# Kernel tuning notes

Measured on AMD Instinct MI355X. Metric: run time of the kernel, lower is better.

Reference implementation:

```python
import jax, jax.numpy as jnp
import numpy as np

NUM_EMBEDDINGS = 16384
EMBED_DIM = 2048
B, C, H, W = 8, EMBED_DIM, 32, 32


def setup_inputs() -> dict:
    key = jax.random.key(0)
    k1, k2 = jax.random.split(key)
    hidden_state = jax.random.normal(k1, (B, C, H, W), dtype=jnp.float32)
    embedding = jax.random.normal(k2, (NUM_EMBEDDINGS, EMBED_DIM), dtype=jnp.float32)
    return {"hidden_state": hidden_state, "embedding": embedding}


def _l2_normalize(x, axis=-1, eps=1e-12):
    # matches torch F.normalize(p=2): x / max(||x||, eps)
    n = jnp.sqrt(jnp.sum(x * x, axis=axis, keepdims=True))
    return x / jnp.maximum(n, eps)


def reference(hidden_state, embedding):
    b, c, h, w = hidden_state.shape
    # (B,C,H,W) -> (B*H*W, C)
    flat = jnp.transpose(hidden_state, (0, 2, 3, 1)).reshape(-1, c)
    z = _l2_normalize(flat)                      # [N, D]
    e = _l2_normalize(embedding)                 # [K, D]
    sim = jnp.matmul(z, e.T)                     # [N, K]
    idx = jnp.argmax(sim, axis=1)                # [N]
    quant = e[idx]                               # [N, D]
    quant = quant.reshape(b, h, w, c).transpose(0, 3, 1, 2)
    return quant, idx
```

## Files before the change

### kernel.cpp

```cpp
#include <hip/hip_runtime.h>
#include <hip/hip_bf16.h>

#define NQ   8192
#define NK   16384
#define DIM  2048
#define KTILES 128
#define QUANT_ELEMS (8*2048*32*32)

typedef __attribute__((ext_vector_type(8))) short bf16x8;
typedef __attribute__((ext_vector_type(4))) float f32x4;

__device__ __forceinline__ void async16(const void* g, void* lds) {
  __builtin_amdgcn_global_load_lds(
      (const __attribute__((address_space(1))) unsigned int*)g,
      (__attribute__((address_space(3))) unsigned int*)lds,
      16, 0, 0);
}

__device__ __forceinline__ void t2_add(float v, int i,
                                       float& v1, int& i1, float& v2, int& i2) {
  if (v > v1) { v2 = v1; i2 = i1; v1 = v; i1 = i; }
  else if (v > v2) { v2 = v; i2 = i; }
}

__global__ __launch_bounds__(256) void norm_e_kernel(
    const float* __restrict__ e, __hip_bfloat16* __restrict__ eh,
    float* __restrict__ enorm) {
  const int k = blockIdx.x;
  const int t = threadIdx.x;
  const float* row = e + (size_t)k * DIM;
  float v[8];
  double ss = 0.0;
#pragma unroll
  for (int j = 0; j < 8; j++) { v[j] = row[t + 256 * j]; ss += (double)v[j] * (double)v[j]; }
  for (int s = 32; s; s >>= 1) ss += __shfl_down(ss, s);
  __shared__ double sb[4];
  __shared__ float snorm;
  if ((t & 63) == 0) sb[t >> 6] = ss;
  __syncthreads();
  if (t == 0) {
    snorm = fmaxf((float)sqrt(sb[0] + sb[1] + sb[2] + sb[3]), 1e-12f);
    enorm[k] = snorm;
  }
  __syncthreads();
  const float nf = snorm;
#pragma unroll
  for (int j = 0; j < 8; j++)
    eh[(size_t)k * DIM + t + 256 * j] = __float2bfloat16(v[j] / nf);
}

__global__ __launch_bounds__(256) void norm_z_kernel(
    const float* __restrict__ hid, __hip_bfloat16* __restrict__ zh) {
  const int bh = blockIdx.x;
  const int b = bh >> 5, h = bh & 31;
  const int n0 = bh * 32;
  const int t = threadIdx.x;
  const int w = t & 31, cp = t >> 5;

  __shared__ double ssq[8][32];
  __shared__ float nrm[32];
  __shared__ float tile[32][65];

  double acc = 0.0;
  const float* base = hid + ((size_t)b * DIM) * 1024 + h * 32 + w;
#pragma unroll 8
  for (int k = 0; k < 256; k++) {
    float val = base[(size_t)(cp * 256 + k) * 1024];
    acc += (double)val * (double)val;
  }
  ssq[cp][w] = acc;
  __syncthreads();
  if (t < 32) {
    double s = 0.0;
#pragma unroll
    for (int j = 0; j < 8; j++) s += ssq[j][t];
    nrm[t] = fmaxf((float)sqrt(s), 1e-12f);
  }
  __syncthreads();

  for (int ct = 0; ct < 32; ct++) {
    const int c0 = ct * 64;
#pragma unroll
    for (int jt = 0; jt < 8; jt++) {
      const int cl = jt * 8 + cp;
      tile[w][cl] = base[(size_t)(c0 + cl) * 1024];
    }
    __syncthreads();
#pragma unroll
    for (int it = 0; it < 8; it++) {
      const int nl = it * 4 + (t >> 6);
      const int cl = t & 63;
      zh[(size_t)(n0 + nl) * DIM + c0 + cl] =
          __float2bfloat16(tile[nl][cl] / nrm[nl]);
    }
    __syncthreads();
  }
}

__global__ __launch_bounds__(512, 2) void gemm_top2(
    const __hip_bfloat16* __restrict__ A, const __hip_bfloat16* __restrict__ B,
    float4* __restrict__ pertile ) {
  __shared__ __align__(16) __hip_bfloat16 As[2][256 * 64];
  __shared__ __align__(16) __hip_bfloat16 Bs[2][256 * 64];

  const int nb = blockIdx.x;
  const int kb = blockIdx.y;
  const int n0 = nb * 256;
  const int k0 = kb * 256;

  const int tid  = threadIdx.x;
  const int wid  = tid >> 6;
  const int lane = tid & 63;
  const int wm = wid >> 2;
  const int wn = wid & 3;

  const int lr = lane >> 3;
  const int sc = ((lane & 7) ^ lr) * 8;
  const int srow = wid * 8 + lr;

  f32x4 acc[8][4];
#pragma unroll
  for (int i = 0; i < 8; i++)
#pragma unroll
    for (int j = 0; j < 4; j++) acc[i][j] = (f32x4){0.f, 0.f, 0.f, 0.f};

#define STAGE(bufi, d0_)                                                      \
  do {                                                                        \
    _Pragma("unroll")                                                         \
    for (int q = 0; q < 4; q++) {                                             \
      const int row = q * 64 + srow;                                          \
      async16(A + (size_t)(n0 + row) * DIM + (d0_) + sc,                      \
              (char*)As[bufi] + q * 8192 + wid * 1024);                       \
      async16(B + (size_t)(k0 + row) * DIM + (d0_) + sc,                      \
              (char*)Bs[bufi] + q * 8192 + wid * 1024);                       \
    }                                                                         \
  } while (0)

#define COMPUTE(bufi)                                                         \
  do {                                                                        \
    _Pragma("unroll")                                                         \
    for (int kk = 0; kk < 2; kk++) {                                          \
      bf16x8 af[8], bfr[4];                                                   \
      const int cg = kk * 4 + (lane >> 4);                                    \
      _Pragma("unroll")                                                       \
      for (int mi = 0; mi < 8; mi++) {                                        \
        int r = wm * 128 + mi * 16 + (lane & 15);                             \
        af[mi] = *(const bf16x8*)(As[bufi] + r * 64 + ((cg ^ (r & 7)) * 8));  \
      }                                                                       \
      _Pragma("unroll")                                                       \
      for (int ni = 0; ni < 4; ni++) {                                        \
        int r = wn * 64 + ni * 16 + (lane & 15);                              \
        bfr[ni] = *(const bf16x8*)(Bs[bufi] + r * 64 + ((cg ^ (r & 7)) * 8)); \
      }                                                                       \
      _Pragma("unroll")                                                       \
      for (int mi = 0; mi < 8; mi++)                                          \
        _Pragma("unroll")                                                     \
        for (int ni = 0; ni < 4; ni++)                                        \
          acc[mi][ni] = __builtin_amdgcn_mfma_f32_16x16x32_bf16(              \
              af[mi], bfr[ni], acc[mi][ni], 0, 0, 0);                         \
    }                                                                         \
  } while (0)

  STAGE(0, 0);
  __syncthreads();
  for (int i = 0; i < 15; i++) {
    const int d0 = i * 128;
    STAGE(1, d0 + 64);
    COMPUTE(0);
    __syncthreads();
    STAGE(0, d0 + 128);
    COMPUTE(1);
    __syncthreads();
  }
  STAGE(1, 1984);
  COMPUTE(0);
  __syncthreads();
  COMPUTE(1);
#undef STAGE
#undef COMPUTE

  __syncthreads();
  float4* buf = (float4*)As;
  const int cbase = k0 + wn * 64 + (lane & 15);
#pragma unroll
  for (int mi = 0; mi < 8; mi++) {
#pragma unroll
    for (int j = 0; j < 4; j++) {
      float v1 = -INFINITY, v2 = -INFINITY;
      int i1 = -1, i2 = -1;
#pragma unroll
      for (int ni = 0; ni < 4; ni++)
        t2_add(acc[mi][ni][j], cbase + ni * 16, v1, i1, v2, i2);
      for (int s = 1; s < 16; s <<= 1) {
        float ov1 = __shfl_xor(v1, s); int oi1 = __shfl_xor(i1, s);
        float ov2 = __shfl_xor(v2, s); int oi2 = __shfl_xor(i2, s);
        t2_add(ov1, oi1, v1, i1, v2, i2);
        t2_add(ov2, oi2, v1, i1, v2, i2);
      }
      if ((lane & 15) == 0) {
        int rl = wm * 128 + mi * 16 + ((lane >> 4) << 2) + j;
        buf[rl * 4 + wn] = make_float4(v1, v2, __int_as_float(i1), __int_as_float(i2));
      }
    }
  }
  __syncthreads();
  {
    const int row = tid >> 1, half = tid & 1;
    float4 a = buf[row * 4 + half * 2 + 0], b = buf[row * 4 + half * 2 + 1];
    float v1 = a.x, v2 = a.y;
    int i1 = __float_as_int(a.z), i2 = __float_as_int(a.w);
    t2_add(b.x, __float_as_int(b.z), v1, i1, v2, i2);
    t2_add(b.y, __float_as_int(b.w), v1, i1, v2, i2);
    pertile[(size_t)(n0 + row) * KTILES + kb * 2 + half] =
        make_float4(v1, v2, __int_as_float(i1), __int_as_float(i2));
  }
}

#define DELTA 2e-3f
__global__ __launch_bounds__(256) void rescore_kernel(
    const float4* __restrict__ pertile, const float* __restrict__ hid,
    const float* __restrict__ emb, float* __restrict__ idx_f,
    int* __restrict__ idx_i) {
  const int n = blockIdx.x;
  const int t = threadIdx.x;
  __shared__ double sredd[2][4];
  __shared__ float sm[4];
  __shared__ int sl[128];
  __shared__ int scnt;

  float4 e4 = (t < 128) ? pertile[(size_t)n * KTILES + t]
                        : make_float4(-INFINITY, -INFINITY, 0.f, 0.f);
  float m = e4.x;
  for (int s = 32; s; s >>= 1) m = fmaxf(m, __shfl_xor(m, s));
  if ((t & 63) == 0) sm[t >> 6] = m;
  __syncthreads();
  if (t == 0) {
    sm[0] = fmaxf(fmaxf(sm[0], sm[1]), fmaxf(sm[2], sm[3]));
    scnt = 0;
  }
  __syncthreads();
  const float thr = sm[0] - DELTA;
  if (t < 128) {
    if (e4.x >= thr) { int p = atomicAdd(&scnt, 1); if (p < 128) sl[p] = __float_as_int(e4.z); }
    if (e4.y >= thr) { int p = atomicAdd(&scnt, 1); if (p < 128) sl[p] = __float_as_int(e4.w); }
  }
  __syncthreads();
  const int cnt = min(scnt, 128);

  const int b = n >> 10, hw = n & 1023;
  const float* zbase = hid + (size_t)b * DIM * 1024 + hw;
  double zv[8];
#pragma unroll
  for (int j = 0; j < 8; j++) zv[j] = (double)zbase[(size_t)(t + 256 * j) * 1024];

  double bestv = -1e300;
  int besti = 0x7fffffff;
  for (int c = 0; c < cnt; c++) {
    const int k = sl[c];
    const float* erow = emb + (size_t)k * DIM;
    double dot = 0.0, ee = 0.0;
#pragma unroll
    for (int j = 0; j < 8; j++) {
      double ev = (double)erow[t + 256 * j];
      dot += zv[j] * ev;
      ee  += ev * ev;
    }
    for (int s = 32; s; s >>= 1) { dot += __shfl_down(dot, s); ee += __shfl_down(ee, s); }
    if ((t & 63) == 0) { sredd[0][t >> 6] = dot; sredd[1][t >> 6] = ee; }
    __syncthreads();
    if (t == 0) {
      double td = sredd[0][0] + sredd[0][1] + sredd[0][2] + sredd[0][3];
      double te = sredd[1][0] + sredd[1][1] + sredd[1][2] + sredd[1][3];
      double sim = td / sqrt(te);
      if (sim > bestv || (sim == bestv && k < besti)) { bestv = sim; besti = k; }
    }
    __syncthreads();
  }
  if (t == 0) { idx_f[n] = (float)besti; idx_i[n] = besti; }
}

__global__ __launch_bounds__(256) void gather_kernel(
    const float* __restrict__ emb, const float* __restrict__ enorm,
    const int* __restrict__ idx, float* __restrict__ out) {
  const int bh = blockIdx.x;
  const int b = bh >> 5, h = bh & 31;
  const int n0 = bh * 32;
  const int c0 = blockIdx.y * 64;
  const int t = threadIdx.x;

  __shared__ int rows[32];
  __shared__ float nrm[32];
  __shared__ float tile[32][65];

  if (t < 32) {
    int r = idx[n0 + t];
    rows[t] = r;
    nrm[t] = enorm[r];
  }
  __syncthreads();
#pragma unroll
  for (int it = 0; it < 8; it++) {
    const int nl = it * 4 + (t >> 6);
    const int cl = t & 63;
    tile[nl][cl] = emb[(size_t)rows[nl] * DIM + c0 + cl] / nrm[nl];
  }
  __syncthreads();
#pragma unroll
  for (int jt = 0; jt < 8; jt++) {
    const int cl = jt * 8 + (t >> 5);
    const int w = t & 31;
    out[((size_t)(b * DIM + c0 + cl) << 10) + (h << 5) + w] = tile[w][cl];
  }
}

extern "C" void kernel_launch(void* const* d_in, const int* in_sizes, int n_in,
                              void* d_out, int out_size, void* d_ws, size_t ws_size,
                              hipStream_t stream) {
  const float* hidden = (const float*)d_in[0];
  const float* emb    = (const float*)d_in[1];
  float* out = (float*)d_out;

  char* ws = (char*)d_ws;
  __hip_bfloat16* eh = (__hip_bfloat16*)ws; ws += (size_t)NK * DIM * 2;
  __hip_bfloat16* zh = (__hip_bfloat16*)ws; ws += (size_t)NQ * DIM * 2;
  float4* pertile = (float4*)ws;            ws += (size_t)NQ * KTILES * 16;
  float* enorm = (float*)ws;                ws += (size_t)NK * 4;
  int* idxi = (int*)ws;                     ws += (size_t)NQ * 4;

  norm_e_kernel<<<NK, 256, 0, stream>>>(emb, eh, enorm);
  norm_z_kernel<<<256, 256, 0, stream>>>(hidden, zh);
  gemm_top2<<<dim3(NQ / 256, NK / 256), 512, 0, stream>>>(zh, eh, pertile);
  rescore_kernel<<<NQ, 256, 0, stream>>>(pertile, hidden, emb, out + QUANT_ELEMS, idxi);
  gather_kernel<<<dim3(256, DIM / 64), 256, 0, stream>>>(emb, enorm, idxi, out);
}
```

Baseline: 2.097 ms.

## Interleave staged global loads with quarter-tile MFMA phases in GEMM main loop

Restructures the bf16 GEMM main loop into four sub-phases per K-tile. Each phase loads a slice of A fragments from LDS, issues part of the next tile's async global-to-LDS copies, then runs a block of MFMAs at raised wave priority. Explicit vmcnt/lgkmcnt waits and raw barriers replace full __syncthreads. The intent is finer-grained overlap of memory traffic with matrix math and lower register pressure from holding fewer A fragments at once. The cost is many more barriers, and hand-tuned wait counts that must match the load order exactly.

```diff
diff --git a/kernel.cpp b/kernel.cpp
--- a/kernel.cpp
+++ b/kernel.cpp
@@ -116,7 +116,12 @@
 
   const int lr = lane >> 3;
   const int sc = ((lane & 7) ^ lr) * 8;
-  const int srow = wid * 8 + lr;
+
+  const int la15 = lane & 15;
+  const int rba  = wm * 128 + la15;
+  const int rbb  = wn * 64 + la15;
+  const int slot0 = (((lane >> 4) ^ (lane & 7)) * 8);
+  const int slot1 = (((4 + (lane >> 4)) ^ (lane & 7)) * 8);
 
   f32x4 acc[8][4];
 #pragma unroll
@@ -124,60 +129,128 @@
 #pragma unroll
     for (int j = 0; j < 4; j++) acc[i][j] = (f32x4){0.f, 0.f, 0.f, 0.f};
 
-#define STAGE(bufi, d0_)                                                      \
+  bf16x8 af[2][2];
+  bf16x8 bfr[4][2];
+
+#define STAGE_BU(BUF, d0_, h)                                                 \
   do {                                                                        \
     _Pragma("unroll")                                                         \
-    for (int q = 0; q < 4; q++) {                                             \
-      const int row = q * 64 + srow;                                          \
-      async16(A + (size_t)(n0 + row) * DIM + (d0_) + sc,                      \
-              (char*)As[bufi] + q * 8192 + wid * 1024);                       \
-      async16(B + (size_t)(k0 + row) * DIM + (d0_) + sc,                      \
-              (char*)Bs[bufi] + q * 8192 + wid * 1024);                       \
+    for (int j_ = 0; j_ < 2; j_++) {                                          \
+      const int row_ = (h) * 128 + j_ * 64 + wid * 8 + lr;                    \
+      async16(B + (size_t)(k0 + row_) * DIM + (d0_) + sc,                     \
+              (char*)&Bs[BUF][0] + (h) * 16384 + j_ * 8192 + wid * 1024);     \
     }                                                                         \
   } while (0)
 
-#define COMPUTE(bufi)                                                         \
+#define STAGE_A1(BUF, d0_, i_)                                                \
+  do {                                                                        \
+    const int row_ = (wid < 4) ? ((i_) * 32 + wid * 8 + lr)                   \
+                               : (128 + (i_) * 32 + (wid - 4) * 8 + lr);      \
+    const int lb_  = (wid < 4) ? ((i_) * 4096 + wid * 1024)                   \
+                               : (16384 + (i_) * 4096 + (wid - 4) * 1024);    \
+    async16(A + (size_t)(n0 + row_) * DIM + (d0_) + sc,                       \
+            (char*)&As[BUF][0] + lb_);                                        \
+  } while (0)
+
+#define AF_LOAD(BUF, q)                                                       \
   do {                                                                        \
     _Pragma("unroll")                                                         \
-    for (int kk = 0; kk < 2; kk++) {                                          \
-      bf16x8 af[8], bfr[4];                                                   \
-      const int cg = kk * 4 + (lane >> 4);                                    \
+    for (int m_ = 0; m_ < 2; m_++) {                                          \
+      af[m_][0] = *(const bf16x8*)(&As[BUF][(rba + (q)*32 + m_*16)*64 + slot0]); \
+      af[m_][1] = *(const bf16x8*)(&As[BUF][(rba + (q)*32 + m_*16)*64 + slot1]); \
+    }                                                                         \
+  } while (0)
+
+#define BF_LOAD(BUF)                                                          \
+  do {                                                                        \
+    _Pragma("unroll")                                                         \
+    for (int n_ = 0; n_ < 4; n_++) {                                          \
+      bfr[n_][0] = *(const bf16x8*)(&Bs[BUF][(rbb + n_*16)*64 + slot0]);      \
+      bfr[n_][1] = *(const bf16x8*)(&Bs[BUF][(rbb + n_*16)*64 + slot1]);      \
+    }                                                                         \
+  } while (0)
+
+#define MFMA_Q(q)                                                             \
+  do {                                                                        \
+    __builtin_amdgcn_s_setprio(1);                                            \
+    _Pragma("unroll")                                                         \
+    for (int kk_ = 0; kk_ < 2; kk_++)                                         \
       _Pragma("unroll")                                                       \
-      for (int mi = 0; mi < 8; mi++) {                                        \
-        int r = wm * 128 + mi * 16 + (lane & 15);                             \
-        af[mi] = *(const bf16x8*)(As[bufi] + r * 64 + ((cg ^ (r & 7)) * 8));  \
-      }                                                                       \
-      _Pragma("unroll")                                                       \
-      for (int ni = 0; ni < 4; ni++) {                                        \
-        int r = wn * 64 + ni * 16 + (lane & 15);                              \
-        bfr[ni] = *(const bf16x8*)(Bs[bufi] + r * 64 + ((cg ^ (r & 7)) * 8)); \
-      }                                                                       \
-      _Pragma("unroll")                                                       \
-      for (int mi = 0; mi < 8; mi++)                                          \
+      for (int m_ = 0; m_ < 2; m_++)                                          \
         _Pragma("unroll")                                                     \
-        for (int ni = 0; ni < 4; ni++)                                        \
-          acc[mi][ni] = __builtin_amdgcn_mfma_f32_16x16x32_bf16(              \
-              af[mi], bfr[ni], acc[mi][ni], 0, 0, 0);                         \
-    }                                                                         \
-  } while (0)
-
-  STAGE(0, 0);
-  __syncthreads();
+        for (int n_ = 0; n_ < 4; n_++)                                        \
+          acc[(q)*2 + m_][n_] = __builtin_amdgcn_mfma_f32_16x16x32_bf16(      \
+              af[m_][kk_], bfr[n_][kk_], acc[(q)*2 + m_][n_], 0, 0, 0);       \
+    __builtin_amdgcn_s_setprio(0);                                            \
+  } while (0)
+
+#define LGKM0 asm volatile("s_waitcnt lgkmcnt(0)" ::: "memory")
+#define BAR   __builtin_amdgcn_s_barrier()
+#define SB0   __builtin_amdgcn_sched_barrier(0)
+
+#define TILE_MAIN(BUF, d0n_)                                                  \
+  do {                                                                        \
+                                                                      \
+    asm volatile("s_waitcnt vmcnt(2)" ::: "memory");                          \
+    BAR;                                                                      \
+    BF_LOAD(BUF); AF_LOAD(BUF, 0);                                            \
+    STAGE_BU(1 - (BUF), (d0n_), 0);                                           \
+    LGKM0; MFMA_Q(0); BAR;                                                    \
+                                                                      \
+    BAR;                                                                      \
+    AF_LOAD(BUF, 1);                                                          \
+    STAGE_BU(1 - (BUF), (d0n_), 1);                                           \
+    LGKM0; MFMA_Q(1); BAR;                                                    \
+                                                                      \
+    asm volatile("s_waitcnt vmcnt(4)" ::: "memory");                          \
+    BAR;                                                                      \
+    AF_LOAD(BUF, 2);                                                          \
+    STAGE_A1(1 - (BUF), (d0n_), 0); STAGE_A1(1 - (BUF), (d0n_), 1);           \
+    LGKM0; MFMA_Q(2); BAR;                                                    \
+                                                                      \
+    BAR;                                                                      \
+    AF_LOAD(BUF, 3);                                                          \
+    STAGE_A1(1 - (BUF), (d0n_), 2); STAGE_A1(1 - (BUF), (d0n_), 3);           \
+    LGKM0; MFMA_Q(3); BAR;                                                    \
+  } while (0)
+
+#define TILE_LAST(BUF)                                                        \
+  do {                                                                        \
+    asm volatile("s_waitcnt vmcnt(2)" ::: "memory");                          \
+    BAR;                                                                      \
+    BF_LOAD(BUF); AF_LOAD(BUF, 0); LGKM0; MFMA_Q(0); BAR;                     \
+    BAR;                                                                      \
+    AF_LOAD(BUF, 1); LGKM0; MFMA_Q(1); BAR;                                   \
+    asm volatile("s_waitcnt vmcnt(0)" ::: "memory");                          \
+    BAR;                                                                      \
+    AF_LOAD(BUF, 2); LGKM0; MFMA_Q(2); BAR;                                   \
+    BAR;                                                                      \
+    AF_LOAD(BUF, 3); LGKM0; MFMA_Q(3); BAR;                                   \
+  } while (0)
+
+  STAGE_BU(0, 0, 0); SB0;
+  STAGE_BU(0, 0, 1); SB0;
+  STAGE_A1(0, 0, 0); STAGE_A1(0, 0, 1); SB0;
+  STAGE_A1(0, 0, 2); STAGE_A1(0, 0, 3);
+
+#pragma unroll 1
   for (int i = 0; i < 15; i++) {
-    const int d0 = i * 128;
-    STAGE(1, d0 + 64);
-    COMPUTE(0);
-    __syncthreads();
-    STAGE(0, d0 + 128);
-    COMPUTE(1);
-    __syncthreads();
-  }
-  STAGE(1, 1984);
-  COMPUTE(0);
-  __syncthreads();
-  COMPUTE(1);
-#undef STAGE
-#undef COMPUTE
+    TILE_MAIN(0, i * 128 + 64);
+    TILE_MAIN(1, i * 128 + 128);
+  }
+  TILE_MAIN(0, 1984);
+  TILE_LAST(1);
+
+#undef TILE_MAIN
+#undef TILE_LAST
+#undef STAGE_BU
+#undef STAGE_A1
+#undef AF_LOAD
+#undef BF_LOAD
+#undef MFMA_Q
+#undef LGKM0
+#undef BAR
+#undef SB0
 
   __syncthreads();
   float4* buf = (float4*)As;
```

After: 1.843 ms. 1.14x faster.

## Halve GEMM K-slab to 32, raise occupancy, use fine-grained vmcnt waits

Applied to the files above, without the earlier changes.

Cuts the per-stage K slab from 64 to 32 so LDS per block halves, and raises launch bounds to 4 blocks per CU. The swizzle is reworked for the narrower rows, and full __syncthreads is replaced by explicit s_waitcnt vmcnt plus s_barrier with sched_barriers. MFMA sections also get setprio, so loads for the next stage overlap compute. The aim is more latency hiding through occupancy and less synchronisation stall. The cost is twice as many barriers per K, and register pressure with 128 accumulator floats at 4 blocks of 512 threads may cause spills.

```diff
diff --git a/kernel.cpp b/kernel.cpp
--- a/kernel.cpp
+++ b/kernel.cpp
@@ -97,11 +97,11 @@
   }
 }
 
-__global__ __launch_bounds__(512, 2) void gemm_top2(
+__global__ __launch_bounds__(512, 4) void gemm_top2(
     const __hip_bfloat16* __restrict__ A, const __hip_bfloat16* __restrict__ B,
     float4* __restrict__ pertile ) {
-  __shared__ __align__(16) __hip_bfloat16 As[2][256 * 64];
-  __shared__ __align__(16) __hip_bfloat16 Bs[2][256 * 64];
+  __shared__ __align__(16) __hip_bfloat16 As[2][256 * 32];
+  __shared__ __align__(16) __hip_bfloat16 Bs[2][256 * 32];
 
   const int nb = blockIdx.x;
   const int kb = blockIdx.y;
@@ -114,9 +114,9 @@
   const int wm = wid >> 2;
   const int wn = wid & 3;
 
-  const int lr = lane >> 3;
-  const int sc = ((lane & 7) ^ lr) * 8;
-  const int srow = wid * 8 + lr;
+  const int la15 = lane & 15;
+  const int slotE = (((lane >> 4) ^ (la15 & 3)) * 8);
+  const int scol = (((lane & 3) ^ ((lane >> 2) & 3)) * 8);
 
   f32x4 acc[8][4];
 #pragma unroll
@@ -124,60 +124,71 @@
 #pragma unroll
     for (int j = 0; j < 4; j++) acc[i][j] = (f32x4){0.f, 0.f, 0.f, 0.f};
 
-#define STAGE(bufi, d0_)                                                      \
+#define STAGE(BUF, d0_)                                                       \
   do {                                                                        \
     _Pragma("unroll")                                                         \
-    for (int q = 0; q < 4; q++) {                                             \
-      const int row = q * 64 + srow;                                          \
-      async16(A + (size_t)(n0 + row) * DIM + (d0_) + sc,                      \
-              (char*)As[bufi] + q * 8192 + wid * 1024);                       \
-      async16(B + (size_t)(k0 + row) * DIM + (d0_) + sc,                      \
-              (char*)Bs[bufi] + q * 8192 + wid * 1024);                       \
+    for (int q_ = 0; q_ < 2; q_++) {                                          \
+      const int row_ = q_ * 128 + wid * 16 + (lane >> 2);                     \
+      async16(A + (size_t)(n0 + row_) * DIM + (d0_) + scol,                   \
+              (char*)&As[BUF][0] + q_ * 8192 + wid * 1024);                   \
+      async16(B + (size_t)(k0 + row_) * DIM + (d0_) + scol,                   \
+              (char*)&Bs[BUF][0] + q_ * 8192 + wid * 1024);                   \
     }                                                                         \
   } while (0)
 
-#define COMPUTE(bufi)                                                         \
+#define COMPUTE(BUF)                                                          \
   do {                                                                        \
+    bf16x8 af[8], bfr[4];                                                     \
     _Pragma("unroll")                                                         \
-    for (int kk = 0; kk < 2; kk++) {                                          \
-      bf16x8 af[8], bfr[4];                                                   \
-      const int cg = kk * 4 + (lane >> 4);                                    \
+    for (int mi = 0; mi < 8; mi++)                                            \
+      af[mi] = *(const bf16x8*)(&As[BUF][(wm * 128 + mi * 16 + la15) * 32 + slotE]); \
+    _Pragma("unroll")                                                         \
+    for (int ni = 0; ni < 4; ni++)                                            \
+      bfr[ni] = *(const bf16x8*)(&Bs[BUF][(wn * 64 + ni * 16 + la15) * 32 + slotE]); \
+    __builtin_amdgcn_s_setprio(1);                                            \
+    _Pragma("unroll")                                                         \
+    for (int mi = 0; mi < 8; mi++)                                            \
       _Pragma("unroll")                                                       \
-      for (int mi = 0; mi < 8; mi++) {                                        \
-        int r = wm * 128 + mi * 16 + (lane & 15);                             \
-        af[mi] = *(const bf16x8*)(As[bufi] + r * 64 + ((cg ^ (r & 7)) * 8));  \
-      }                                                                       \
-      _Pragma("unroll")                                                       \
-      for (int ni = 0; ni < 4; ni++) {                                        \
-        int r = wn * 64 + ni * 16 + (lane & 15);                              \
-        bfr[ni] = *(const bf16x8*)(Bs[bufi] + r * 64 + ((cg ^ (r & 7)) * 8)); \
-      }                                                                       \
-      _Pragma("unroll")                                                       \
-      for (int mi = 0; mi < 8; mi++)                                          \
-        _Pragma("unroll")                                                     \
-        for (int ni = 0; ni < 4; ni++)                                        \
-          acc[mi][ni] = __builtin_amdgcn_mfma_f32_16x16x32_bf16(              \
-              af[mi], bfr[ni], acc[mi][ni], 0, 0, 0);                         \
-    }                                                                         \
+      for (int ni = 0; ni < 4; ni++)                                          \
+        acc[mi][ni] = __builtin_amdgcn_mfma_f32_16x16x32_bf16(                \
+            af[mi], bfr[ni], acc[mi][ni], 0, 0, 0);                           \
+    __builtin_amdgcn_s_setprio(0);                                            \
   } while (0)
 
+#define VMCNT4 asm volatile("s_waitcnt vmcnt(4)" ::: "memory")
+#define VMCNT0 asm volatile("s_waitcnt vmcnt(0)" ::: "memory")
+#define BAR    __builtin_amdgcn_s_barrier()
+#define SB0    __builtin_amdgcn_sched_barrier(0)
+
   STAGE(0, 0);
-  __syncthreads();
-  for (int i = 0; i < 15; i++) {
-    const int d0 = i * 128;
-    STAGE(1, d0 + 64);
+#pragma unroll 1
+  for (int i = 0; i < 31; i++) {
+    const int d0 = i * 64;
+    STAGE(1, d0 + 32);
+    VMCNT4;
+    BAR; SB0;
     COMPUTE(0);
-    __syncthreads();
-    STAGE(0, d0 + 128);
+    BAR; SB0;
+    STAGE(0, d0 + 64);
+    VMCNT4;
+    BAR; SB0;
     COMPUTE(1);
-    __syncthreads();
-  }
-  STAGE(1, 1984);
+    BAR; SB0;
+  }
+  STAGE(1, 2016);
+  VMCNT4;
+  BAR; SB0;
   COMPUTE(0);
-  __syncthreads();
+  VMCNT0;
+  BAR; SB0;
   COMPUTE(1);
+
 #undef STAGE
 #undef COMPUTE
+#undef VMCNT4
+#undef VMCNT0
+#undef BAR
+#undef SB0
 
   __syncthreads();
   float4* buf = (float4*)As;
```

New measurement: 6.526 ms. 211% more time.
